# Kernel optimization log

Measured on AMD Instinct MI355X. Metric: run time of the kernel, lower is better.

The kernel has to match this reference:

```python
import jax, jax.numpy as jnp
import numpy as np

B, T, D, H, E = 4, 2048, 1024, 2048, 8
TOP_K = int(E * 0.25)  # = 2


def setup_inputs() -> dict:
    key = jax.random.key(0)
    ks = jax.random.split(key, 6)
    x = jax.random.normal(ks[0], (B, T, D), dtype=jnp.float32)
    gate = jax.random.normal(ks[1], (D, E), dtype=jnp.float32)
    # per-expert 2-layer MLP params (D -> H -> D), stacked over experts
    W1 = jax.random.normal(ks[2], (E, D, H), dtype=jnp.float32) * (D ** -0.5)
    b1 = jnp.zeros((E, H), dtype=jnp.float32)
    W2 = jax.random.normal(ks[3], (E, H, D), dtype=jnp.float32) * (H ** -0.5)
    b2 = jnp.zeros((E, D), dtype=jnp.float32)
    return {"x": x, "gate": gate, "W1": W1, "b1": b1, "W2": W2, "b2": b2}


def reference(x, gate, W1, b1, W2, b2):
    # gating: softmax over experts, then top-k mask, renormalize (L1 over experts)
    raw_gate = jax.nn.softmax(jnp.einsum('btd,de->bte', x, gate), axis=-1)  # [B,T,E]
    topk_scores, topk_idx = jax.lax.top_k(raw_gate, TOP_K)                   # [B,T,k]
    mask = jax.nn.one_hot(topk_idx, E, dtype=raw_gate.dtype).sum(axis=-2)    # [B,T,E]
    gate_topk = mask * raw_gate
    gate_topk = gate_topk / jnp.maximum(gate_topk.sum(axis=-1, keepdims=True), 1e-12)
    # dense all-expert compute (faithful to the original: every expert sees every token)
    h = jax.nn.relu(jnp.einsum('btd,edh->beth', x, W1) + b1[None, :, None, :])  # [B,E,T,H]
    expert_out = jnp.einsum('beth,ehd->betd', h, W2) + b2[None, :, None, :]     # [B,E,T,D]
    # weighted combine
    out = jnp.einsum('bte,betd->btd', gate_topk, expert_out)  # [B,T,D]
    return out
```

## Files before the change

kernel.cpp:

```cpp
#include <hip/hip_runtime.h>

#define E_      8
#define D_      1024
#define H_      2048
#define TOKENS  8192
#define RROWS   16384
#define HPAD_ROWS (RROWS + 128)

using bf16x8 = __attribute__((ext_vector_type(8))) __bf16;
using f32x4  = __attribute__((ext_vector_type(4))) float;

__device__ __forceinline__ unsigned short f2bf(float f) {
  unsigned u = __builtin_bit_cast(unsigned, f);
  u += 0x7fffu + ((u >> 16) & 1u);
  return (unsigned short)(u >> 16);
}
__device__ __forceinline__ float bf2f(unsigned short u) {
  unsigned v = (unsigned)u << 16;
  return __builtin_bit_cast(float, v);
}

#define GLDS16(g, l) __builtin_amdgcn_global_load_lds( \
    (const __attribute__((address_space(1))) unsigned int*)(g), \
    (__attribute__((address_space(3))) unsigned int*)(l), 16, 0, 0)

#define SBAR() asm volatile("s_barrier" ::: "memory")


__global__ void transpose_cvt_kernel(const float* __restrict__ src,
                                     unsigned short* __restrict__ dst,
                                     int R, int C) {
  int tilesC = C >> 6, tilesR = R >> 6;
  int per = tilesR * tilesC;
  int b = blockIdx.x;
  int e = b / per, rem = b % per;
  int rb = rem / tilesC, cb = rem % tilesC;
  __shared__ float tile[64][65];
  const float* s = src + (size_t)e * R * C;
  unsigned short* d = dst + (size_t)e * R * C;
  int r0 = rb << 6, c0 = cb << 6;
#pragma unroll
  for (int i = 0; i < 16; i++) {
    int idx = threadIdx.x + i * 256;
    int lr = idx >> 6, lc = idx & 63;
    tile[lr][lc] = s[(size_t)(r0 + lr) * C + (c0 + lc)];
  }
  __syncthreads();
#pragma unroll
  for (int i = 0; i < 16; i++) {
    int idx = threadIdx.x + i * 256;
    int lr = idx >> 6, lc = idx & 63;
    d[(size_t)(c0 + lr) * R + (r0 + lc)] = f2bf(tile[lc][lr]);
  }
}

__global__ void gating_kernel(const float* __restrict__ x, const float* __restrict__ gate,
                              unsigned short* __restrict__ xb,
                              int* __restrict__ sel, float* __restrict__ wsel) {
  int lane = threadIdx.x & 63, wid = threadIdx.x >> 6;
  int t = (blockIdx.x << 2) + wid;
  const float* xr = x + (size_t)t * D_;
  unsigned short* xbr = xb + (size_t)t * D_;
  float acc[8];
#pragma unroll
  for (int e = 0; e < 8; e++) acc[e] = 0.f;
#pragma unroll
  for (int i = 0; i < 4; i++) {
    int d0 = (i << 8) + (lane << 2);
    float4 xv = *reinterpret_cast<const float4*>(xr + d0);
    ushort4 o = make_ushort4(f2bf(xv.x), f2bf(xv.y), f2bf(xv.z), f2bf(xv.w));
    *reinterpret_cast<ushort4*>(xbr + d0) = o;
    float xa[4] = {xv.x, xv.y, xv.z, xv.w};
#pragma unroll
    for (int j = 0; j < 4; j++) {
      const float4* g4 = reinterpret_cast<const float4*>(gate + (size_t)(d0 + j) * 8);
      float4 ga = g4[0], gb = g4[1];
      acc[0] += xa[j] * ga.x; acc[1] += xa[j] * ga.y;
      acc[2] += xa[j] * ga.z; acc[3] += xa[j] * ga.w;
      acc[4] += xa[j] * gb.x; acc[5] += xa[j] * gb.y;
      acc[6] += xa[j] * gb.z; acc[7] += xa[j] * gb.w;
    }
  }
#pragma unroll
  for (int e = 0; e < 8; e++) {
#pragma unroll
    for (int off = 32; off; off >>= 1) acc[e] += __shfl_xor(acc[e], off);
  }
  if (lane == 0) {
    int i0 = 0; float v0 = acc[0];
#pragma unroll
    for (int e = 1; e < 8; e++) if (acc[e] > v0) { v0 = acc[e]; i0 = e; }
    int i1 = -1; float v1 = -3.4e38f;
#pragma unroll
    for (int e = 0; e < 8; e++) if (e != i0 && acc[e] > v1) { v1 = acc[e]; i1 = e; }
    float p1 = expf(v1 - v0);
    float inv = 1.f / (1.f + p1);
    sel[t * 2] = i0; sel[t * 2 + 1] = i1;
    wsel[t * 2] = inv; wsel[t * 2 + 1] = p1 * inv;
  }
}

__global__ __launch_bounds__(1024) void route_kernel(
    const int* __restrict__ sel, int* __restrict__ cnt, int* __restrict__ off,
    int* __restrict__ tok_id, int* __restrict__ pos) {
  const int tid = threadIdx.x;
  const int lane = tid & 63, wid = tid >> 6;
  __shared__ int wtot[16][8];
  __shared__ int woff[16][8];
  __shared__ int offs[8];
  int sv[16];
  const int s0 = tid << 4;
#pragma unroll
  for (int q = 0; q < 4; q++) {
    int4 v = reinterpret_cast<const int4*>(sel + s0)[q];
    sv[q * 4 + 0] = v.x; sv[q * 4 + 1] = v.y;
    sv[q * 4 + 2] = v.z; sv[q * 4 + 3] = v.w;
  }
  int h[8];
#pragma unroll
  for (int e = 0; e < 8; e++) h[e] = 0;
#pragma unroll
  for (int j = 0; j < 16; j++) {
    int ev = sv[j];
#pragma unroll
    for (int e = 0; e < 8; e++) h[e] += (ev == e) ? 1 : 0;
  }
  int excl[8];
#pragma unroll
  for (int e = 0; e < 8; e++) {
    int v = h[e];
#pragma unroll
    for (int d = 1; d < 64; d <<= 1) {
      int u = __shfl_up(v, d);
      if (lane >= d) v += u;
    }
    excl[e] = v - h[e];
    if (lane == 63) wtot[wid][e] = v;
  }
  __syncthreads();
  if (tid == 0) {
    int run[8];
#pragma unroll
    for (int e = 0; e < 8; e++) run[e] = 0;
    for (int w = 0; w < 16; w++)
#pragma unroll
      for (int e = 0; e < 8; e++) { woff[w][e] = run[e]; run[e] += wtot[w][e]; }
    int a = 0;
    for (int e = 0; e < 8; e++) { offs[e] = a; off[e] = a; cnt[e] = run[e]; a += run[e]; }
  }
  __syncthreads();
  int base[8];
#pragma unroll
  for (int e = 0; e < 8; e++) base[e] = offs[e] + woff[wid][e] + excl[e];
#pragma unroll
  for (int j = 0; j < 16; j++) {
    int ev = sv[j];
    int p = 0;
#pragma unroll
    for (int e = 0; e < 8; e++) if (ev == e) { p = base[e]; base[e] = p + 1; }
    pos[s0 + j] = p;
    tok_id[p] = (s0 + j) >> 1;
  }
}


#define STAGE_T(slot, kh) do { \
  const size_t ko = (size_t)(kh) << 7; \
  _Pragma("unroll") \
  for (int i = 0; i < 4; i++) { \
    GLDS16(Ab + gA[i] + ko, &Asm[slot][((wid << 2) + i) << 9]); \
    GLDS16(Bb + gB[i] + ko, &Bsm[slot][((wid << 2) + i) << 9]); \
  } \
} while (0)

__global__ __launch_bounds__(256, 2) void gemm1_kernel(
    const unsigned short* __restrict__ xb,
    const unsigned short* __restrict__ w1t,
    const float* __restrict__ b1,
    unsigned short* __restrict__ hbuf,
    const int* __restrict__ tok_id,
    const int* __restrict__ cnt, const int* __restrict__ off) {
  const int nwg = E_ * 64 * 16;
  const int raw = blockIdx.x;
  const int bid = (raw & 7) * (nwg >> 3) + (raw >> 3);
  const int e  = bid >> 10;
  const int rb = (bid >> 4) & 63;
  const int cb = bid & 15;
  const int rows = cnt[e];
  const int m0 = rb << 7;
  if (m0 >= rows) return;
  const int base = off[e];
  const int tid = threadIdx.x, lane = tid & 63, wid = tid >> 6;
  const int wr = wid >> 1, wc = wid & 1;

  __shared__ __align__(16) unsigned short Asm[2][128 * 64];
  __shared__ __align__(16) unsigned short Bsm[2][128 * 64];

  const int c8 = lane & 7, r8 = lane >> 3;
  const size_t swz = (size_t)((c8 ^ r8) << 4);
  size_t gA[4], gB[4];
  const int n0 = cb << 7;
#pragma unroll
  for (int i = 0; i < 4; i++) {
    int r = ((wid << 2) + i) << 3;
    int ar = m0 + r + r8; if (ar >= rows) ar = rows - 1;
    gA[i] = (size_t)tok_id[base + ar] * (D_ * 2) + swz;
    gB[i] = (size_t)(n0 + r + r8) * (D_ * 2) + swz;
  }
  const char* Ab = (const char*)xb;
  const char* Bb = (const char*)w1t + (size_t)e * H_ * D_ * 2;

  const int aRow = ((wr << 6) + (lane & 15)) * 128;
  const int bRow = ((wc << 6) + (lane & 15)) * 128;
  const int cby0 = (((lane >> 4)) ^ (lane & 7)) << 4;
  const int cby1 = ((4 + (lane >> 4)) ^ (lane & 7)) << 4;

  f32x4 acc[4][4] = {};
  const int KH = D_ / 64;

  STAGE_T(0, 0);
  STAGE_T(1, 1);
  asm volatile("s_waitcnt vmcnt(8)" ::: "memory");
  SBAR();

  for (int kh = 0; kh < KH; ++kh) {
    const int cur = kh & 1;
    const char* Ap = (const char*)&Asm[cur][0] + aRow;
    const char* Bp = (const char*)&Bsm[cur][0] + bRow;
    bf16x8 a[4], b[4], a2[4], b2[4];
#pragma unroll
    for (int m = 0; m < 4; m++) a[m]  = *(const bf16x8*)(Ap + cby0 + m * 2048);
#pragma unroll
    for (int n = 0; n < 4; n++) b[n]  = *(const bf16x8*)(Bp + cby0 + n * 2048);
#pragma unroll
    for (int m = 0; m < 4; m++) a2[m] = *(const bf16x8*)(Ap + cby1 + m * 2048);
#pragma unroll
    for (int n = 0; n < 4; n++) b2[n] = *(const bf16x8*)(Bp + cby1 + n * 2048);
    asm volatile("s_waitcnt lgkmcnt(0)" ::: "memory");
    __builtin_amdgcn_sched_barrier(0);
    SBAR();
    if (kh + 2 < KH) STAGE_T(cur, kh + 2);
    __builtin_amdgcn_s_setprio(1);
#pragma unroll
    for (int m = 0; m < 4; m++)
#pragma unroll
      for (int n = 0; n < 4; n++)
        acc[m][n] = __builtin_amdgcn_mfma_f32_16x16x32_bf16(a[m], b[n], acc[m][n], 0, 0, 0);
#pragma unroll
    for (int m = 0; m < 4; m++)
#pragma unroll
      for (int n = 0; n < 4; n++)
        acc[m][n] = __builtin_amdgcn_mfma_f32_16x16x32_bf16(a2[m], b2[n], acc[m][n], 0, 0, 0);
    __builtin_amdgcn_s_setprio(0);
    if (kh + 2 < KH) {
      asm volatile("s_waitcnt vmcnt(8)" ::: "memory");
    } else if (kh + 1 < KH) {
      asm volatile("s_waitcnt vmcnt(0)" ::: "memory");
    }
    SBAR();
  }

  const int rcnt = rows - m0;
  const float* b1e = b1 + e * H_;
#pragma unroll
  for (int m = 0; m < 4; m++) {
#pragma unroll
    for (int q = 0; q < 4; q++) {
      int rl = (wr << 6) + (m << 4) + ((lane >> 4) << 2) + q;
      if (rl < rcnt) {
        unsigned short* hrow = hbuf + (size_t)(base + m0 + rl) * H_;
#pragma unroll
        for (int n = 0; n < 4; n++) {
          int ncol = n0 + (wc << 6) + (n << 4) + (lane & 15);
          float v = acc[m][n][q] + b1e[ncol];
          hrow[ncol] = f2bf(fmaxf(v, 0.f));
        }
      }
    }
  }
}

__global__ __launch_bounds__(256, 2) void gemm2_kernel(
    const unsigned short* __restrict__ hbuf,
    const unsigned short* __restrict__ w2t,
    unsigned short* __restrict__ eout,
    const int* __restrict__ cnt, const int* __restrict__ off) {
  const int nwg = E_ * 64 * 8;
  const int raw = blockIdx.x;
  const int bid = (raw & 7) * (nwg >> 3) + (raw >> 3);
  const int e  = bid >> 9;
  const int rb = (bid >> 3) & 63;
  const int cb = bid & 7;
  const int rows = cnt[e];
  const int m0 = rb << 7;
  if (m0 >= rows) return;
  const int base = off[e];
  const int tid = threadIdx.x, lane = tid & 63, wid = tid >> 6;
  const int wr = wid >> 1, wc = wid & 1;

  __shared__ __align__(16) unsigned short Asm[2][128 * 64];
  __shared__ __align__(16) unsigned short Bsm[2][128 * 64];

  const int c8 = lane & 7, r8 = lane >> 3;
  const size_t swz = (size_t)((c8 ^ r8) << 4);
  size_t gA[4], gB[4];
  const int n0 = cb << 7;
#pragma unroll
  for (int i = 0; i < 4; i++) {
    int r = ((wid << 2) + i) << 3;
    gA[i] = (size_t)(base + m0 + r + r8) * (H_ * 2) + swz;
    gB[i] = (size_t)(n0 + r + r8) * (H_ * 2) + swz;
  }
  const char* Ab = (const char*)hbuf;
  const char* Bb = (const char*)w2t + (size_t)e * D_ * H_ * 2;

  const int aRow = ((wr << 6) + (lane & 15)) * 128;
  const int bRow = ((wc << 6) + (lane & 15)) * 128;
  const int cby0 = (((lane >> 4)) ^ (lane & 7)) << 4;
  const int cby1 = ((4 + (lane >> 4)) ^ (lane & 7)) << 4;

  f32x4 acc[4][4] = {};
  const int KH = H_ / 64;

  STAGE_T(0, 0);
  STAGE_T(1, 1);
  asm volatile("s_waitcnt vmcnt(8)" ::: "memory");
  SBAR();

  for (int kh = 0; kh < KH; ++kh) {
    const int cur = kh & 1;
    const char* Ap = (const char*)&Asm[cur][0] + aRow;
    const char* Bp = (const char*)&Bsm[cur][0] + bRow;
    bf16x8 a[4], b[4], a2[4], b2[4];
#pragma unroll
    for (int m = 0; m < 4; m++) a[m]  = *(const bf16x8*)(Ap + cby0 + m * 2048);
#pragma unroll
    for (int n = 0; n < 4; n++) b[n]  = *(const bf16x8*)(Bp + cby0 + n * 2048);
#pragma unroll
    for (int m = 0; m < 4; m++) a2[m] = *(const bf16x8*)(Ap + cby1 + m * 2048);
#pragma unroll
    for (int n = 0; n < 4; n++) b2[n] = *(const bf16x8*)(Bp + cby1 + n * 2048);
    asm volatile("s_waitcnt lgkmcnt(0)" ::: "memory");
    __builtin_amdgcn_sched_barrier(0);
    SBAR();
    if (kh + 2 < KH) STAGE_T(cur, kh + 2);
    __builtin_amdgcn_s_setprio(1);
#pragma unroll
    for (int m = 0; m < 4; m++)
#pragma unroll
      for (int n = 0; n < 4; n++)
        acc[m][n] = __builtin_amdgcn_mfma_f32_16x16x32_bf16(a[m], b[n], acc[m][n], 0, 0, 0);
#pragma unroll
    for (int m = 0; m < 4; m++)
#pragma unroll
      for (int n = 0; n < 4; n++)
        acc[m][n] = __builtin_amdgcn_mfma_f32_16x16x32_bf16(a2[m], b2[n], acc[m][n], 0, 0, 0);
    __builtin_amdgcn_s_setprio(0);
    if (kh + 2 < KH) {
      asm volatile("s_waitcnt vmcnt(8)" ::: "memory");
    } else if (kh + 1 < KH) {
      asm volatile("s_waitcnt vmcnt(0)" ::: "memory");
    }
    SBAR();
  }

  const int rcnt = rows - m0;
#pragma unroll
  for (int m = 0; m < 4; m++) {
#pragma unroll
    for (int q = 0; q < 4; q++) {
      int rl = (wr << 6) + (m << 4) + ((lane >> 4) << 2) + q;
      if (rl < rcnt) {
        unsigned short* erow = eout + (size_t)(base + m0 + rl) * D_;
#pragma unroll
        for (int n = 0; n < 4; n++) {
          int ncol = n0 + (wc << 6) + (n << 4) + (lane & 15);
          erow[ncol] = f2bf(acc[m][n][q]);
        }
      }
    }
  }
}

__global__ void combine_kernel(const unsigned short* __restrict__ eout,
                               const float* __restrict__ b2,
                               const int* __restrict__ sel, const float* __restrict__ wsel,
                               const int* __restrict__ pos,
                               float* __restrict__ out) {
  int t = blockIdx.x;
  int d = threadIdx.x << 2;
  int e0 = sel[t * 2], e1 = sel[t * 2 + 1];
  float w0 = wsel[t * 2], w1 = wsel[t * 2 + 1];
  int p0 = pos[t * 2], p1 = pos[t * 2 + 1];
  ushort4 y0 = *reinterpret_cast<const ushort4*>(eout + (size_t)p0 * D_ + d);
  ushort4 y1 = *reinterpret_cast<const ushort4*>(eout + (size_t)p1 * D_ + d);
  float4 c0 = *reinterpret_cast<const float4*>(b2 + (size_t)e0 * D_ + d);
  float4 c1 = *reinterpret_cast<const float4*>(b2 + (size_t)e1 * D_ + d);
  float4 o;
  o.x = w0 * (bf2f(y0.x) + c0.x) + w1 * (bf2f(y1.x) + c1.x);
  o.y = w0 * (bf2f(y0.y) + c0.y) + w1 * (bf2f(y1.y) + c1.y);
  o.z = w0 * (bf2f(y0.z) + c0.z) + w1 * (bf2f(y1.z) + c1.z);
  o.w = w0 * (bf2f(y0.w) + c0.w) + w1 * (bf2f(y1.w) + c1.w);
  *reinterpret_cast<float4*>(out + (size_t)t * D_ + d) = o;
}


extern "C" void kernel_launch(void* const* d_in, const int* in_sizes, int n_in,
                              void* d_out, int out_size, void* d_ws, size_t ws_size,
                              hipStream_t stream) {
  (void)in_sizes; (void)n_in; (void)ws_size; (void)out_size;
  const float* x    = (const float*)d_in[0];
  const float* gate = (const float*)d_in[1];
  const float* W1   = (const float*)d_in[2];
  const float* b1   = (const float*)d_in[3];
  const float* W2   = (const float*)d_in[4];
  const float* b2   = (const float*)d_in[5];
  float* out = (float*)d_out;

  char* p = (char*)d_ws;
  unsigned short* xb   = (unsigned short*)p; p += (size_t)TOKENS * D_ * 2;
  unsigned short* w1t  = (unsigned short*)p; p += (size_t)E_ * H_ * D_ * 2;
  unsigned short* w2t  = (unsigned short*)p; p += (size_t)E_ * D_ * H_ * 2;
  unsigned short* hbuf = (unsigned short*)p; p += (size_t)HPAD_ROWS * H_ * 2;
  int*   tok  = (int*)p;   p += (size_t)RROWS * 4;
  int*   pos  = (int*)p;   p += (size_t)TOKENS * 2 * 4;
  int*   sel  = (int*)p;   p += (size_t)TOKENS * 2 * 4;
  float* wsel = (float*)p; p += (size_t)TOKENS * 2 * 4;
  int* cnt    = (int*)p;   p += 32 * 4;
  int* off    = (int*)p;   p += 32 * 4;
  unsigned short* eout = w1t;

  transpose_cvt_kernel<<<E_ * (D_ / 64) * (H_ / 64), 256, 0, stream>>>(W1, w1t, D_, H_);
  transpose_cvt_kernel<<<E_ * (H_ / 64) * (D_ / 64), 256, 0, stream>>>(W2, w2t, H_, D_);
  gating_kernel<<<TOKENS / 4, 256, 0, stream>>>(x, gate, xb, sel, wsel);
  route_kernel<<<1, 1024, 0, stream>>>(sel, cnt, off, tok, pos);
  gemm1_kernel<<<E_ * 64 * 16, 256, 0, stream>>>(xb, w1t, b1, hbuf, tok, cnt, off);
  gemm2_kernel<<<E_ * 64 * 8, 256, 0, stream>>>(hbuf, w2t, eout, cnt, off);
  combine_kernel<<<TOKENS, 256, 0, stream>>>(eout, b2, sel, wsel, pos, out);
}
```

Baseline: 299.1 us.

## Merge weight transposes, split A/B staging across MFMA halves, widen combine

```diff
diff --git a/kernel.cpp b/kernel.cpp
--- a/kernel.cpp
+++ b/kernel.cpp
@@ -27,12 +27,17 @@
 #define SBAR() asm volatile("s_barrier" ::: "memory")
 
 
-__global__ void transpose_cvt_kernel(const float* __restrict__ src,
-                                     unsigned short* __restrict__ dst,
-                                     int R, int C) {
-  int tilesC = C >> 6, tilesR = R >> 6;
-  int per = tilesR * tilesC;
+__global__ void transpose_cvt2_kernel(const float* __restrict__ W1,
+                                      unsigned short* __restrict__ w1t,
+                                      const float* __restrict__ W2,
+                                      unsigned short* __restrict__ w2t) {
   int b = blockIdx.x;
+  const int nb1 = E_ * (D_ >> 6) * (H_ >> 6);
+  const float* src; unsigned short* dst; int R, C;
+  if (b < nb1) { src = W1; dst = w1t; R = D_; C = H_; }
+  else         { src = W2; dst = w2t; R = H_; C = D_; b -= nb1; }
+  int tilesC = C >> 6;
+  int per = (R >> 6) * tilesC;
   int e = b / per, rem = b % per;
   int rb = rem / tilesC, cb = rem % tilesC;
   __shared__ float tile[64][65];
@@ -164,13 +169,17 @@
 }
 
 
-#define STAGE_T(slot, kh) do { \
+#define STAGE_A(slot, kh) do { \
   const size_t ko = (size_t)(kh) << 7; \
   _Pragma("unroll") \
-  for (int i = 0; i < 4; i++) { \
+  for (int i = 0; i < 4; i++) \
     GLDS16(Ab + gA[i] + ko, &Asm[slot][((wid << 2) + i) << 9]); \
+} while (0)
+#define STAGE_B(slot, kh) do { \
+  const size_t ko = (size_t)(kh) << 7; \
+  _Pragma("unroll") \
+  for (int i = 0; i < 4; i++) \
     GLDS16(Bb + gB[i] + ko, &Bsm[slot][((wid << 2) + i) << 9]); \
-  } \
 } while (0)
 
 __global__ __launch_bounds__(256, 2) void gemm1_kernel(
@@ -218,8 +227,8 @@
   f32x4 acc[4][4] = {};
   const int KH = D_ / 64;
 
-  STAGE_T(0, 0);
-  STAGE_T(1, 1);
+  STAGE_A(0, 0); STAGE_B(0, 0);
+  STAGE_A(1, 1); STAGE_B(1, 1);
   asm volatile("s_waitcnt vmcnt(8)" ::: "memory");
   SBAR();
 
@@ -239,13 +248,16 @@
     asm volatile("s_waitcnt lgkmcnt(0)" ::: "memory");
     __builtin_amdgcn_sched_barrier(0);
     SBAR();
-    if (kh + 2 < KH) STAGE_T(cur, kh + 2);
+    if (kh + 2 < KH) STAGE_A(cur, kh + 2);
     __builtin_amdgcn_s_setprio(1);
 #pragma unroll
     for (int m = 0; m < 4; m++)
 #pragma unroll
       for (int n = 0; n < 4; n++)
         acc[m][n] = __builtin_amdgcn_mfma_f32_16x16x32_bf16(a[m], b[n], acc[m][n], 0, 0, 0);
+    __builtin_amdgcn_s_setprio(0);
+    if (kh + 2 < KH) STAGE_B(cur, kh + 2);
+    __builtin_amdgcn_s_setprio(1);
 #pragma unroll
     for (int m = 0; m < 4; m++)
 #pragma unroll
@@ -322,8 +334,8 @@
   f32x4 acc[4][4] = {};
   const int KH = H_ / 64;
 
-  STAGE_T(0, 0);
-  STAGE_T(1, 1);
+  STAGE_A(0, 0); STAGE_B(0, 0);
+  STAGE_A(1, 1); STAGE_B(1, 1);
   asm volatile("s_waitcnt vmcnt(8)" ::: "memory");
   SBAR();
 
@@ -343,13 +355,16 @@
     asm volatile("s_waitcnt lgkmcnt(0)" ::: "memory");
     __builtin_amdgcn_sched_barrier(0);
     SBAR();
-    if (kh + 2 < KH) STAGE_T(cur, kh + 2);
+    if (kh + 2 < KH) STAGE_A(cur, kh + 2);
     __builtin_amdgcn_s_setprio(1);
 #pragma unroll
     for (int m = 0; m < 4; m++)
 #pragma unroll
       for (int n = 0; n < 4; n++)
         acc[m][n] = __builtin_amdgcn_mfma_f32_16x16x32_bf16(a[m], b[n], acc[m][n], 0, 0, 0);
+    __builtin_amdgcn_s_setprio(0);
+    if (kh + 2 < KH) STAGE_B(cur, kh + 2);
+    __builtin_amdgcn_s_setprio(1);
 #pragma unroll
     for (int m = 0; m < 4; m++)
 #pragma unroll
@@ -387,21 +402,30 @@
                                const int* __restrict__ sel, const float* __restrict__ wsel,
                                const int* __restrict__ pos,
                                float* __restrict__ out) {
-  int t = blockIdx.x;
-  int d = threadIdx.x << 2;
+  int t = (blockIdx.x << 2) + (threadIdx.x >> 6);
+  int lane = threadIdx.x & 63;
   int e0 = sel[t * 2], e1 = sel[t * 2 + 1];
   float w0 = wsel[t * 2], w1 = wsel[t * 2 + 1];
   int p0 = pos[t * 2], p1 = pos[t * 2 + 1];
-  ushort4 y0 = *reinterpret_cast<const ushort4*>(eout + (size_t)p0 * D_ + d);
-  ushort4 y1 = *reinterpret_cast<const ushort4*>(eout + (size_t)p1 * D_ + d);
-  float4 c0 = *reinterpret_cast<const float4*>(b2 + (size_t)e0 * D_ + d);
-  float4 c1 = *reinterpret_cast<const float4*>(b2 + (size_t)e1 * D_ + d);
-  float4 o;
-  o.x = w0 * (bf2f(y0.x) + c0.x) + w1 * (bf2f(y1.x) + c1.x);
-  o.y = w0 * (bf2f(y0.y) + c0.y) + w1 * (bf2f(y1.y) + c1.y);
-  o.z = w0 * (bf2f(y0.z) + c0.z) + w1 * (bf2f(y1.z) + c1.z);
-  o.w = w0 * (bf2f(y0.w) + c0.w) + w1 * (bf2f(y1.w) + c1.w);
-  *reinterpret_cast<float4*>(out + (size_t)t * D_ + d) = o;
+  const unsigned short* y0r = eout + (size_t)p0 * D_;
+  const unsigned short* y1r = eout + (size_t)p1 * D_;
+  const float* c0r = b2 + (size_t)e0 * D_;
+  const float* c1r = b2 + (size_t)e1 * D_;
+  float* orow = out + (size_t)t * D_;
+#pragma unroll
+  for (int j = 0; j < 4; j++) {
+    int d = (j << 8) + (lane << 2);
+    ushort4 y0 = *reinterpret_cast<const ushort4*>(y0r + d);
+    ushort4 y1 = *reinterpret_cast<const ushort4*>(y1r + d);
+    float4 c0 = *reinterpret_cast<const float4*>(c0r + d);
+    float4 c1 = *reinterpret_cast<const float4*>(c1r + d);
+    float4 o;
+    o.x = w0 * (bf2f(y0.x) + c0.x) + w1 * (bf2f(y1.x) + c1.x);
+    o.y = w0 * (bf2f(y0.y) + c0.y) + w1 * (bf2f(y1.y) + c1.y);
+    o.z = w0 * (bf2f(y0.z) + c0.z) + w1 * (bf2f(y1.z) + c1.z);
+    o.w = w0 * (bf2f(y0.w) + c0.w) + w1 * (bf2f(y1.w) + c1.w);
+    *reinterpret_cast<float4*>(orow + d) = o;
+  }
 }
 
 
@@ -430,11 +454,12 @@
   int* off    = (int*)p;   p += 32 * 4;
   unsigned short* eout = w1t;
 
-  transpose_cvt_kernel<<<E_ * (D_ / 64) * (H_ / 64), 256, 0, stream>>>(W1, w1t, D_, H_);
-  transpose_cvt_kernel<<<E_ * (H_ / 64) * (D_ / 64), 256, 0, stream>>>(W2, w2t, H_, D_);
+  const int nb1 = E_ * (D_ / 64) * (H_ / 64);
+  const int nb2 = E_ * (H_ / 64) * (D_ / 64);
+  transpose_cvt2_kernel<<<nb1 + nb2, 256, 0, stream>>>(W1, w1t, W2, w2t);
   gating_kernel<<<TOKENS / 4, 256, 0, stream>>>(x, gate, xb, sel, wsel);
   route_kernel<<<1, 1024, 0, stream>>>(sel, cnt, off, tok, pos);
   gemm1_kernel<<<E_ * 64 * 16, 256, 0, stream>>>(xb, w1t, b1, hbuf, tok, cnt, off);
   gemm2_kernel<<<E_ * 64 * 8, 256, 0, stream>>>(hbuf, w2t, eout, cnt, off);
-  combine_kernel<<<TOKENS, 256, 0, stream>>>(eout, b2, sel, wsel, pos, out);
-}
+  combine_kernel<<<TOKENS / 4, 256, 0, stream>>>(eout, b2, sel, wsel, pos, out);
+}
```

Measured after the change: 295.1 us. No clear change (-1.3%).
